# Optimization experiments

Measured on AMD Instinct MI355X. Metric: run time of the kernel, lower is better.

Reference implementation:

```python
import jax, jax.numpy as jnp
import numpy as np

EPS = 1e-05


def setup_inputs() -> dict:
    key = jax.random.key(0)
    k1, k2, k3, k4, k5 = jax.random.split(key, 5)
    B, Cin, T = 8, 512, 4096
    K, N, D = 8, 2048, 256
    return {
        "embeddings": jax.random.normal(k1, (B, Cin, T), dtype=jnp.float32),
        "w_in": jax.random.normal(k2, (D, Cin), dtype=jnp.float32) * 0.05,
        "w_out": jax.random.normal(k3, (Cin, D), dtype=jnp.float32) * 0.05,
        "embed_sum": jax.random.normal(k4, (K, N, D), dtype=jnp.float32),
        "cluster_usage": jax.random.uniform(k5, (K, N), dtype=jnp.float32, minval=0.5, maxval=1.5),
    }


def reference(embeddings, w_in, w_out, embed_sum, cluster_usage):
    # input_proj: 1x1 conv == channel matmul. [B, 512, T] -> [B, T, 256]
    x = jnp.einsum("dc,bct->btd", w_in, embeddings)
    # per-quantizer codebooks: embed_sum / clamp(cluster_usage)  -> [K, N, D]
    embeds = embed_sum / jnp.clip(cluster_usage, EPS, None)[..., None]

    def step(residual, embed):
        # squared-euclidean distance (same argmin as cdist p=2)
        # dists: [B, T, N]
        d = (
            jnp.sum(residual * residual, axis=-1, keepdims=True)
            - 2.0 * jnp.einsum("btd,nd->btn", residual, embed)
            + jnp.sum(embed * embed, axis=-1)
        )
        idx = jnp.argmin(d, axis=-1)          # [B, T] int
        q = embed[idx]                        # gather -> [B, T, D]
        return residual - q, (idx, q)

    _, (codes, qs) = jax.lax.scan(step, x, embeds)
    # codes: [K, B, T]; qs: [K, B, T, D]
    quantized = jnp.sum(qs, axis=0)           # decode: sum over quantizers
    out = jnp.einsum("cd,btd->bct", w_out, quantized)  # output_proj -> [B, 512, T]
    return codes, out
```

## Files before the change

### kernel.cpp

```cpp
#include <hip/hip_runtime.h>
#include <float.h>
#include <math.h>

#define EPSF 1e-5f
#define NRM_BIAS 2048.0f

constexpr int B_  = 8;
constexpr int CIN = 512;
constexpr int T_  = 4096;
constexpr int K_  = 8;
constexpr int N_  = 2048;
constexpr int D_  = 256;
constexpr int BT  = B_ * T_;

typedef _Float16 v8h __attribute__((ext_vector_type(8)));
typedef _Float16 v4h __attribute__((ext_vector_type(4)));
typedef float    v4f __attribute__((ext_vector_type(4)));

static __device__ __forceinline__ unsigned umn(unsigned a, unsigned b) { return a < b ? a : b; }
static __device__ __forceinline__ unsigned umx(unsigned a, unsigned b) { return a > b ? a : b; }

__global__ void __launch_bounds__(256) prep_kernel(const float* __restrict__ embed_sum,
                                                   const float* __restrict__ usage,
                                                   float* __restrict__ inv,
                                                   float* __restrict__ nrm,
                                                   _Float16* __restrict__ ehs) {
  int w    = threadIdx.x >> 6;
  int lane = threadIdx.x & 63;
  int kn   = blockIdx.x * 4 + w;
  int k    = kn >> 11, n = kn & (N_ - 1);
  const float* s = embed_sum + (size_t)kn * D_;
  float um = fmaxf(usage[kn], EPSF);
  float4 sv = *(const float4*)(s + lane * 4);
  float e0 = sv.x / um, e1 = sv.y / um, e2 = sv.z / um, e3 = sv.w / um;
  float v = e0 * e0 + e1 * e1 + e2 * e2 + e3 * e3;

  int half = n >> 10, chunk = (n >> 4) & 63, r = n & 15;
  int cg = lane >> 1, sub = lane & 1;
  v4h h4; h4[0] = (_Float16)e0; h4[1] = (_Float16)e1;
  h4[2] = (_Float16)e2; h4[3] = (_Float16)e3;
  size_t off16 = ((size_t)((k * 2 + half) * 64 + chunk)) * 4096
               + (size_t)(cg * 16 + r) * 8 + (size_t)sub * 4;
  *(v4h*)(ehs + off16) = h4;

  for (int off = 32; off > 0; off >>= 1) v += __shfl_down(v, off);
  if (lane == 0) { inv[kn] = 1.0f / um; nrm[kn] = v + NRM_BIAS; }
}

__global__ void __launch_bounds__(64) wprep_x_kernel(const float* __restrict__ w_in,
                                                     v8h* __restrict__ afragX) {
  int lane = threadIdx.x;
  int mt = blockIdx.x >> 4, kstep = blockIdx.x & 15;
  int m = mt * 16 + (lane & 15), k0 = kstep * 32 + (lane >> 4) * 8;
  const float* src = w_in + (size_t)m * CIN + k0;
  float4 f0 = *(const float4*)src, f1 = *(const float4*)(src + 4);
  float e[8] = {f0.x, f0.y, f0.z, f0.w, f1.x, f1.y, f1.z, f1.w};
  v8h h, l;
#pragma unroll
  for (int j = 0; j < 8; j++) {
    _Float16 hh = (_Float16)e[j];
    h[j] = hh; l[j] = (_Float16)(e[j] - (float)hh);
  }
  v8h* dst = afragX + ((size_t)blockIdx.x * 64 + lane) * 2;
  dst[0] = h; dst[1] = l;
}

__global__ void __launch_bounds__(256) wc_kernel(const float* __restrict__ w_out,
                                                 const float* __restrict__ w_in,
                                                 float* __restrict__ wc) {
  int c  = blockIdx.x >> 1;
  int cp = (blockIdx.x & 1) * 256 + threadIdx.x;
  float acc = 0.f;
  for (int d = 0; d < D_; d++)
    acc += w_out[(size_t)c * D_ + d] * w_in[(size_t)d * CIN + cp];
  wc[(size_t)c * CIN + cp] = acc;
}

__global__ void __launch_bounds__(64) wprep_o_kernel(const float* __restrict__ wc,
                                                     const float* __restrict__ w_out,
                                                     v8h* __restrict__ afragO) {
  int lane = threadIdx.x;
  int mt = blockIdx.x / 24, kstep = blockIdx.x % 24;
  int m = mt * 16 + (lane & 15), k0 = kstep * 32 + (lane >> 4) * 8;
  float e[8];
  if (k0 < CIN) {
    const float* s = wc + (size_t)m * CIN + k0;
#pragma unroll
    for (int j = 0; j < 8; j++) e[j] = s[j];
  } else {
    const float* s = w_out + (size_t)m * D_ + (k0 - CIN);
#pragma unroll
    for (int j = 0; j < 8; j++) e[j] = -s[j];
  }
  v8h h, l;
#pragma unroll
  for (int j = 0; j < 8; j++) {
    _Float16 hh = (_Float16)e[j];
    h[j] = hh; l[j] = (_Float16)(e[j] - (float)hh);
  }
  v8h* dst = afragO + ((size_t)blockIdx.x * 64 + lane) * 2;
  dst[0] = h; dst[1] = l;
}

__global__ void __launch_bounds__(256, 4) proj_x_kernel(const float* __restrict__ emb,
                                                        const v8h* __restrict__ afragX,
                                                        float* __restrict__ rb) {
  int tid = threadIdx.x, wave = tid >> 6, lane = tid & 63;
  int lr = lane & 15, lg = lane >> 4;
  int tb = blockIdx.x >> 1, nb = blockIdx.x & 1;
  int t0 = tb * 64 + wave * 16;
  int b  = t0 >> 12;
  const float* ebase = emb + (size_t)b * CIN * T_ + (t0 & (T_ - 1)) + lr;

  v4f acc[8];
#pragma unroll
  for (int nt = 0; nt < 8; nt++) acc[nt] = (v4f){0.f, 0.f, 0.f, 0.f};

  for (int ks = 0; ks < 16; ks++) {
    float e[8];
#pragma unroll
    for (int j = 0; j < 8; j++)
      e[j] = ebase[(size_t)(ks * 32 + lg * 8 + j) * T_];
    v8h Eh, El;
#pragma unroll
    for (int j = 0; j < 8; j++) {
      _Float16 hh = (_Float16)e[j];
      Eh[j] = hh; El[j] = (_Float16)(e[j] - (float)hh);
    }
    const v8h* ap = afragX + ((size_t)ks * 64 + lane) * 2;
#pragma unroll
    for (int nt = 0; nt < 8; nt++) {
      int mt = nb * 8 + nt;
      v8h Wh = ap[(size_t)mt * 2048];
      v8h Wl = ap[(size_t)mt * 2048 + 1];
      acc[nt] = __builtin_amdgcn_mfma_f32_16x16x32_f16(Eh, Wh, acc[nt], 0, 0, 0);
      acc[nt] = __builtin_amdgcn_mfma_f32_16x16x32_f16(El, Wh, acc[nt], 0, 0, 0);
      acc[nt] = __builtin_amdgcn_mfma_f32_16x16x32_f16(Eh, Wl, acc[nt], 0, 0, 0);
    }
  }
#pragma unroll
  for (int nt = 0; nt < 8; nt++)
#pragma unroll
    for (int r = 0; r < 4; r++)
      rb[(size_t)(t0 + lg * 4 + r) * D_ + (nb * 8 + nt) * 16 + lr] = acc[nt][r];
}

__global__ void __launch_bounds__(256, 4) proj_out_kernel(const float* __restrict__ emb,
                                                          const float* __restrict__ rb,
                                                          const v8h* __restrict__ afragO,
                                                          float* __restrict__ outb) {
  int tid = threadIdx.x, wave = tid >> 6, lane = tid & 63;
  int lr = lane & 15, lg = lane >> 4;
  int tb = blockIdx.x >> 1, mb = blockIdx.x & 1;
  int t0 = tb * 64 + wave * 16;
  int b  = t0 >> 12;
  const float* ebase = emb + (size_t)b * CIN * T_ + (t0 & (T_ - 1)) + lr;

  v4f acc[16];
#pragma unroll
  for (int mt = 0; mt < 16; mt++) acc[mt] = (v4f){0.f, 0.f, 0.f, 0.f};

  for (int ks = 0; ks < 24; ks++) {
    float e[8];
    if (ks < 16) {
#pragma unroll
      for (int j = 0; j < 8; j++)
        e[j] = ebase[(size_t)(ks * 32 + lg * 8 + j) * T_];
    } else {
      const float* rrow = rb + (size_t)(t0 + lr) * D_ + (ks - 16) * 32 + lg * 8;
      float4 f0 = *(const float4*)rrow, f1 = *(const float4*)(rrow + 4);
      e[0] = f0.x; e[1] = f0.y; e[2] = f0.z; e[3] = f0.w;
      e[4] = f1.x; e[5] = f1.y; e[6] = f1.z; e[7] = f1.w;
    }
    v8h Bh;
#pragma unroll
    for (int j = 0; j < 8; j++) Bh[j] = (_Float16)e[j];
#pragma unroll
    for (int mt = 0; mt < 16; mt++) {
      v8h Ah = afragO[(((size_t)(mb * 16 + mt) * 24 + ks) * 64 + lane) * 2];
      acc[mt] = __builtin_amdgcn_mfma_f32_16x16x32_f16(Ah, Bh, acc[mt], 0, 0, 0);
    }
  }
  float* op = outb + (size_t)b * CIN * T_ + (t0 & (T_ - 1)) + lr;
#pragma unroll
  for (int mt = 0; mt < 16; mt++)
#pragma unroll
    for (int r = 0; r < 4; r++)
      op[(size_t)((mt + mb * 16) * 16 + lg * 4 + r) * T_] = acc[mt][r];
}

__device__ __forceinline__ void merge_save(unsigned b1[4], unsigned b2[4], unsigned b3[4],
                                           int half, int wave, int lg, int lr,
                                           int (*candL)[6]) {
#pragma unroll
  for (int rI = 0; rI < 4; rI++) {
    unsigned k1 = b1[rI], k2 = b2[rI], k3 = b3[rI];
    int n1 = (int)(k1 & 127u) * 16 + lr;
    int n2 = (int)(k2 & 127u) * 16 + lr;
    int n3 = (int)(k3 & 127u) * 16 + lr;
    int o0 = 0, o1 = 0, o2v = 0;
#pragma unroll
    for (int round = 0; round < 3; round++) {
      unsigned mk = k1; int mn = n1;
#pragma unroll
      for (int st = 1; st < 16; st <<= 1) {
        unsigned ok = (unsigned)__shfl_xor((int)mk, st);
        int      on = __shfl_xor(mn, st);
        bool t = (ok < mk) || (ok == mk && on < mn);
        mk = t ? ok : mk; mn = t ? on : mn;
      }
      if (round == 0) o0 = mn; else if (round == 1) o1 = mn; else o2v = mn;
      bool own = (k1 == mk) && (n1 == mn);
      k1 = own ? k2 : k1; n1 = own ? n2 : n1;
      k2 = own ? k3 : k2; n2 = own ? n3 : n2;
      k3 = own ? 0xFFFFFFFFu : k3; n3 = own ? 0x7fffffff : n3;
    }
    if (lr == 0) {
      int* cp = candL[wave * 16 + lg * 4 + rI] + half * 3;
      cp[0] = o0; cp[1] = o1; cp[2] = o2v;
    }
  }
}

__global__ void __launch_bounds__(512)
__attribute__((amdgpu_waves_per_eu(2, 2)))
rvq_mega_kernel(const _Float16* __restrict__ ehs,
                const float* __restrict__ nrm,
                const float* __restrict__ inv_,
                const float* __restrict__ usage,
                const float* __restrict__ embed_sum,
                float* __restrict__ rb,
                float* __restrict__ codes_f) {
  __shared__ v8h ldsB[2][2048];
  __shared__ int candL[128][6];

  int tid  = threadIdx.x;
  int wave = tid >> 6, lane = tid & 63;
  int lr = lane & 15, lg = lane >> 4;
  int wbase = blockIdx.x * 128 + wave * 16;
  int token = wbase + lr;

  float r64[64];
  {
    const float* rrow = rb + (size_t)token * D_ + lg * 8;
#pragma unroll
    for (int c = 0; c < 8; c++) {
      float4 f0 = *(const float4*)(rrow + c * 32);
      float4 f1 = *(const float4*)(rrow + c * 32 + 4);
      r64[c * 8 + 0] = f0.x; r64[c * 8 + 1] = f0.y;
      r64[c * 8 + 2] = f0.z; r64[c * 8 + 3] = f0.w;
      r64[c * 8 + 4] = f1.x; r64[c * 8 + 5] = f1.y;
      r64[c * 8 + 6] = f1.z; r64[c * 8 + 7] = f1.w;
    }
  }

  for (int k = 0; k < K_; k++) {
    v8h A[8];
#pragma unroll
    for (int c = 0; c < 8; c++) {
      v8h a;
#pragma unroll
      for (int j = 0; j < 8; j++) a[j] = (_Float16)r64[c * 8 + j];
      A[c] = a;
    }

    const v8h* src = (const v8h*)(ehs + (size_t)k * 2 * (64 * 4096));

#pragma unroll
    for (int q = 0; q < 4; q++) {
      int idx = tid + q * 512;
      __builtin_amdgcn_global_load_lds(
          (__attribute__((address_space(1))) void*)(void*)(src + idx),
          (__attribute__((address_space(3))) void*)(&ldsB[0][idx]), 16, 0, 0);
    }

    unsigned b1[4], b2[4], b3[4];
#pragma unroll
    for (int i = 0; i < 4; i++) { b1[i] = b2[i] = b3[i] = 0xFFFFFFFFu; }
    const float* nrm_k = nrm + (size_t)k * N_;
    __syncthreads();

    for (int g = 0; g < 32; g++) {
      int cur = g & 1;
      if (g + 1 < 32) {
        const v8h* gsrc = src + (size_t)(g + 1) * 2048;
#pragma unroll
        for (int q = 0; q < 4; q++) {
          int idx = tid + q * 512;
          __builtin_amdgcn_global_load_lds(
              (__attribute__((address_space(1))) void*)(void*)(gsrc + idx),
              (__attribute__((address_space(3))) void*)(&ldsB[cur ^ 1][idx]), 16, 0, 0);
        }
      }

      v4f acc[4];
#pragma unroll
      for (int m = 0; m < 4; m++) acc[m] = (v4f){0.f, 0.f, 0.f, 0.f};
#pragma unroll
      for (int c = 0; c < 8; c++) {
#pragma unroll
        for (int m = 0; m < 4; m++) {
          v8h Bf = ldsB[cur][m * 512 + (c * 4 + lg) * 16 + lr];
          acc[m] = __builtin_amdgcn_mfma_f32_16x16x32_f16(A[c], Bf, acc[m], 0, 0, 0);
        }
      }
#pragma unroll
      for (int m = 0; m < 4; m++) {
        unsigned cg = (unsigned)(4 * g + m);
        float nv = nrm_k[cg * 16 + lr];
#pragma unroll
        for (int j = 0; j < 4; j++) {
          float s = fmaf(-2.0f, acc[m][j], nv);
          unsigned pk = (__float_as_uint(s) & 0xFFFFFF80u) | cg;
          unsigned t = umx(b1[j], pk);
          unsigned u = umx(b2[j], pk);
          b1[j] = umn(b1[j], pk);
          b2[j] = umn(b2[j], t);
          b3[j] = umn(b3[j], u);
        }
      }
      if (g == 15) {
        merge_save(b1, b2, b3, 0, wave, lg, lr, candL);
#pragma unroll
        for (int i = 0; i < 4; i++) { b1[i] = b2[i] = b3[i] = 0xFFFFFFFFu; }
      }
      __syncthreads();
    }
    merge_save(b1, b2, b3, 1, wave, lg, lr, candL);
    __syncthreads();

    const float* es_k  = embed_sum + (size_t)k * N_ * D_;
    const float* us_k  = usage + (size_t)k * N_;
    const float* inv_k = inv_  + (size_t)k * N_;

    int c6[6];
#pragma unroll
    for (int i = 0; i < 6; i++) c6[i] = candL[wave * 16 + lr][i];

    float dots[6];
#pragma unroll
    for (int i = 0; i < 6; i++) {
      const float* sr = es_k + (size_t)c6[i] * D_ + lg * 8;
      float a = 0.f;
#pragma unroll
      for (int c = 0; c < 8; c++) {
        float4 s0 = *(const float4*)(sr + c * 32);
        float4 s1 = *(const float4*)(sr + c * 32 + 4);
        a += r64[c * 8 + 0] * s0.x + r64[c * 8 + 1] * s0.y
           + r64[c * 8 + 2] * s0.z + r64[c * 8 + 3] * s0.w
           + r64[c * 8 + 4] * s1.x + r64[c * 8 + 5] * s1.y
           + r64[c * 8 + 6] * s1.z + r64[c * 8 + 7] * s1.w;
      }
      dots[i] = a;
    }
#pragma unroll
    for (int i = 0; i < 6; i++) {
      dots[i] += __shfl_xor(dots[i], 16);
      dots[i] += __shfl_xor(dots[i], 32);
    }

    float bs = FLT_MAX, bv2 = FLT_MAX; int bn = 0x7fffffff, bn2 = 0x7fffffff;
#pragma unroll
    for (int i = 0; i < 6; i++) {
      int n = c6[i];
      float s = nrm_k[n] - 2.0f * inv_k[n] * dots[i];
      bool better = (s < bs) || (s == bs && n < bn);
      bool second = (s < bv2) || (s == bv2 && n < bn2);
      if (better)      { bv2 = bs; bn2 = bn; bs = s; bn = n; }
      else if (second) { bv2 = s;  bn2 = n; }
    }
    int winner = bn;
    if (bv2 - bs < 0.5f && bn2 != bn) {
      double sc[2]; int nn[2] = { bn, bn2 };
#pragma unroll
      for (int cI = 0; cI < 2; cI++) {
        double u = fmax((double)us_k[nn[cI]], 1e-5);
        double uinv = 1.0 / u;
        const float* srow = es_k + (size_t)nn[cI] * D_ + lg * 8;
        double dotre = 0.0, ee = 0.0;
#pragma unroll
        for (int c = 0; c < 8; c++) {
          float4 s0 = *(const float4*)(srow + c * 32);
          float4 s1 = *(const float4*)(srow + c * 32 + 4);
          double e0 = (double)s0.x * uinv, e1 = (double)s0.y * uinv;
          double e2 = (double)s0.z * uinv, e3 = (double)s0.w * uinv;
          double e4 = (double)s1.x * uinv, e5 = (double)s1.y * uinv;
          double e6 = (double)s1.z * uinv, e7 = (double)s1.w * uinv;
          dotre += (double)r64[c * 8 + 0] * e0 + (double)r64[c * 8 + 1] * e1
                 + (double)r64[c * 8 + 2] * e2 + (double)r64[c * 8 + 3] * e3
                 + (double)r64[c * 8 + 4] * e4 + (double)r64[c * 8 + 5] * e5
                 + (double)r64[c * 8 + 6] * e6 + (double)r64[c * 8 + 7] * e7;
          ee += e0 * e0 + e1 * e1 + e2 * e2 + e3 * e3
              + e4 * e4 + e5 * e5 + e6 * e6 + e7 * e7;
        }
        dotre += __shfl_xor(dotre, 16); dotre += __shfl_xor(dotre, 32);
        ee    += __shfl_xor(ee, 16);    ee    += __shfl_xor(ee, 32);
        sc[cI] = ee - 2.0 * dotre;
      }
      if (sc[1] < sc[0] || (sc[1] == sc[0] && nn[1] < nn[0])) winner = nn[1];
    }

    float um = fmaxf(us_k[winner], EPSF);
    const float* sw = es_k + (size_t)winner * D_ + lg * 8;
#pragma unroll
    for (int c = 0; c < 8; c++) {
      float4 s0 = *(const float4*)(sw + c * 32);
      float4 s1 = *(const float4*)(sw + c * 32 + 4);
      r64[c * 8 + 0] -= s0.x / um; r64[c * 8 + 1] -= s0.y / um;
      r64[c * 8 + 2] -= s0.z / um; r64[c * 8 + 3] -= s0.w / um;
      r64[c * 8 + 4] -= s1.x / um; r64[c * 8 + 5] -= s1.y / um;
      r64[c * 8 + 6] -= s1.z / um; r64[c * 8 + 7] -= s1.w / um;
    }
    if (lg == 0) codes_f[(size_t)k * BT + token] = (float)winner;
  }

  {
    float* wrow = rb + (size_t)token * D_ + lg * 8;
#pragma unroll
    for (int c = 0; c < 8; c++) {
      float4 f0 = make_float4(r64[c * 8 + 0], r64[c * 8 + 1],
                              r64[c * 8 + 2], r64[c * 8 + 3]);
      float4 f1 = make_float4(r64[c * 8 + 4], r64[c * 8 + 5],
                              r64[c * 8 + 6], r64[c * 8 + 7]);
      *(float4*)(wrow + c * 32)     = f0;
      *(float4*)(wrow + c * 32 + 4) = f1;
    }
  }
}

extern "C" void kernel_launch(void* const* d_in, const int* in_sizes, int n_in,
                              void* d_out, int out_size, void* d_ws, size_t ws_size,
                              hipStream_t stream) {
  const float* emb       = (const float*)d_in[0];
  const float* w_in      = (const float*)d_in[1];
  const float* w_out     = (const float*)d_in[2];
  const float* embed_sum = (const float*)d_in[3];
  const float* usage     = (const float*)d_in[4];

  float* outp    = (float*)d_out;
  float* codes_f = outp;
  float* proj_o  = outp + (size_t)K_ * BT;

  float* rb   = (float*)d_ws;
  float* inv  = rb + (size_t)BT * D_;
  float* nrm  = inv + (size_t)K_ * N_;
  int*   cand = (int*)(nrm + (size_t)K_ * N_);
  _Float16* ehs = (_Float16*)(cand + (size_t)BT * 6);
  v8h* afragX = (v8h*)(ehs + (size_t)K_ * N_ * D_);
  float* wc   = (float*)(afragX + 16 * 16 * 64 * 2);
  v8h* afragO = (v8h*)(wc + 512 * 512);

  hipLaunchKernelGGL(wprep_x_kernel, dim3(256), dim3(64), 0, stream, w_in, afragX);
  hipLaunchKernelGGL(wc_kernel, dim3(1024), dim3(256), 0, stream, w_out, w_in, wc);
  hipLaunchKernelGGL(wprep_o_kernel, dim3(768), dim3(64), 0, stream, wc, w_out, afragO);
  hipLaunchKernelGGL(prep_kernel, dim3(K_ * N_ / 4), dim3(256), 0, stream,
                     embed_sum, usage, inv, nrm, ehs);
  hipLaunchKernelGGL(proj_x_kernel, dim3(BT / 32), dim3(256), 0, stream,
                     emb, afragX, rb);
  hipLaunchKernelGGL(rvq_mega_kernel, dim3(BT / 128), dim3(512), 0, stream,
                     ehs, nrm, inv, usage, embed_sum, rb, codes_f);
  hipLaunchKernelGGL(proj_out_kernel, dim3(BT / 32), dim3(256), 0, stream,
                     emb, rb, afragO, proj_o);
}
```

Baseline: 869.3 us.

## Triple-buffer codebook LDS tiles with partial vmcnt waits and raw barriers

```diff
diff --git a/kernel.cpp b/kernel.cpp
--- a/kernel.cpp
+++ b/kernel.cpp
@@ -223,7 +223,6 @@
 }
 
 __global__ void __launch_bounds__(512)
-__attribute__((amdgpu_waves_per_eu(2, 2)))
 rvq_mega_kernel(const _Float16* __restrict__ ehs,
                 const float* __restrict__ nrm,
                 const float* __restrict__ inv_,
@@ -231,7 +230,7 @@
                 const float* __restrict__ embed_sum,
                 float* __restrict__ rb,
                 float* __restrict__ codes_f) {
-  __shared__ v8h ldsB[2][2048];
+  __shared__ v8h ldsB[3][2048];
   __shared__ int candL[128][6];
 
   int tid  = threadIdx.x;
@@ -265,6 +264,11 @@
     }
 
     const v8h* src = (const v8h*)(ehs + (size_t)k * 2 * (64 * 4096));
+    const float* nrm_k = nrm + (size_t)k * N_;
+
+    unsigned b1[4], b2[4], b3[4];
+#pragma unroll
+    for (int i = 0; i < 4; i++) { b1[i] = b2[i] = b3[i] = 0xFFFFFFFFu; }
 
 #pragma unroll
     for (int q = 0; q < 4; q++) {
@@ -273,23 +277,29 @@
           (__attribute__((address_space(1))) void*)(void*)(src + idx),
           (__attribute__((address_space(3))) void*)(&ldsB[0][idx]), 16, 0, 0);
     }
-
-    unsigned b1[4], b2[4], b3[4];
-#pragma unroll
-    for (int i = 0; i < 4; i++) { b1[i] = b2[i] = b3[i] = 0xFFFFFFFFu; }
-    const float* nrm_k = nrm + (size_t)k * N_;
-    __syncthreads();
-
-    for (int g = 0; g < 32; g++) {
-      int cur = g & 1;
-      if (g + 1 < 32) {
-        const v8h* gsrc = src + (size_t)(g + 1) * 2048;
+#pragma unroll
+    for (int q = 0; q < 4; q++) {
+      int idx = tid + q * 512;
+      __builtin_amdgcn_global_load_lds(
+          (__attribute__((address_space(1))) void*)(void*)(src + 2048 + idx),
+          (__attribute__((address_space(3))) void*)(&ldsB[1][idx]), 16, 0, 0);
+    }
+    asm volatile("s_waitcnt vmcnt(4) lgkmcnt(0)" ::: "memory");
+    __builtin_amdgcn_sched_barrier(0);
+    __builtin_amdgcn_s_barrier();
+    __builtin_amdgcn_sched_barrier(0);
+
+    for (int g = 0; g < 30; g++) {
+      int cur = g % 3;
+      {
+        const v8h* gsrc = src + (size_t)(g + 2) * 2048;
+        v8h* dst = ldsB[(g + 2) % 3];
 #pragma unroll
         for (int q = 0; q < 4; q++) {
           int idx = tid + q * 512;
           __builtin_amdgcn_global_load_lds(
               (__attribute__((address_space(1))) void*)(void*)(gsrc + idx),
-              (__attribute__((address_space(3))) void*)(&ldsB[cur ^ 1][idx]), 16, 0, 0);
+              (__attribute__((address_space(3))) void*)(&dst[idx]), 16, 0, 0);
         }
       }
 
@@ -310,8 +320,8 @@
         float nv = nrm_k[cg * 16 + lr];
 #pragma unroll
         for (int j = 0; j < 4; j++) {
-          float s = fmaf(-2.0f, acc[m][j], nv);
-          unsigned pk = (__float_as_uint(s) & 0xFFFFFF80u) | cg;
+          float sv = fmaf(-2.0f, acc[m][j], nv);
+          unsigned pk = (__float_as_uint(sv) & 0xFFFFFF80u) | cg;
           unsigned t = umx(b1[j], pk);
           unsigned u = umx(b2[j], pk);
           b1[j] = umn(b1[j], pk);
@@ -323,6 +333,40 @@
         merge_save(b1, b2, b3, 0, wave, lg, lr, candL);
 #pragma unroll
         for (int i = 0; i < 4; i++) { b1[i] = b2[i] = b3[i] = 0xFFFFFFFFu; }
+      }
+      asm volatile("s_waitcnt vmcnt(4) lgkmcnt(0)" ::: "memory");
+      __builtin_amdgcn_sched_barrier(0);
+      __builtin_amdgcn_s_barrier();
+      __builtin_amdgcn_sched_barrier(0);
+    }
+
+    for (int g = 30; g < 32; g++) {
+      int cur = g % 3;
+      v4f acc[4];
+#pragma unroll
+      for (int m = 0; m < 4; m++) acc[m] = (v4f){0.f, 0.f, 0.f, 0.f};
+#pragma unroll
+      for (int c = 0; c < 8; c++) {
+#pragma unroll
+        for (int m = 0; m < 4; m++) {
+          v8h Bf = ldsB[cur][m * 512 + (c * 4 + lg) * 16 + lr];
+          acc[m] = __builtin_amdgcn_mfma_f32_16x16x32_f16(A[c], Bf, acc[m], 0, 0, 0);
+        }
+      }
+#pragma unroll
+      for (int m = 0; m < 4; m++) {
+        unsigned cg = (unsigned)(4 * g + m);
+        float nv = nrm_k[cg * 16 + lr];
+#pragma unroll
+        for (int j = 0; j < 4; j++) {
+          float sv = fmaf(-2.0f, acc[m][j], nv);
+          unsigned pk = (__float_as_uint(sv) & 0xFFFFFF80u) | cg;
+          unsigned t = umx(b1[j], pk);
+          unsigned u = umx(b2[j], pk);
+          b1[j] = umn(b1[j], pk);
+          b2[j] = umn(b2[j], t);
+          b3[j] = umn(b3[j], u);
+        }
       }
       __syncthreads();
     }
```

After: 848.0 us. -2.4%, faster.
